# Optimization experiments

Hardware: AMD Instinct MI355X
Metric: run time of the kernel (lower is better)

The kernel has to match this reference:

```python
import jax, jax.numpy as jnp
import numpy as np

N_NODES = 10000
IN_SIZE, H_SIZE, OUT_SIZE = 512, 512, 64
N_EDGES = 163840


def gcn_conv(x, edge_index, W, b, n_nodes):
    """PyG-style GCNConv: add self-loops, sym-normalize, x @ W, scatter-add, + bias."""
    src, dst = edge_index[0], edge_index[1]
    loop = jnp.arange(n_nodes, dtype=src.dtype)
    src = jnp.concatenate([src, loop])
    dst = jnp.concatenate([dst, loop])
    # degree over destinations (self-loops included)
    deg = jax.ops.segment_sum(jnp.ones_like(dst, dtype=x.dtype), dst, num_segments=n_nodes)
    dinv = jnp.where(deg > 0, jax.lax.rsqrt(deg), 0.0)
    norm = dinv[src] * dinv[dst]                      # [E+N]
    h = x @ W                                          # [N, out]
    msg = h[src] * norm[:, None]                       # gather + scale
    out = jax.ops.segment_sum(msg, dst, num_segments=n_nodes)  # scatter-add
    return out + b


def setup_inputs() -> dict:
    key = jax.random.key(0)
    k = jax.random.split(key, 6)
    x = jax.random.normal(k[0], (N_NODES, IN_SIZE), dtype=jnp.float32)
    edge_index = jax.random.randint(k[1], (2, N_EDGES), 0, N_NODES, dtype=jnp.int64 if jax.config.read('jax_enable_x64') else jnp.int32)
    # Glorot-ish init for weights, zero bias (PyG default)
    W1 = jax.random.normal(k[2], (IN_SIZE, H_SIZE), dtype=jnp.float32) * (1.0 / np.sqrt(IN_SIZE))
    b1 = jnp.zeros((H_SIZE,), dtype=jnp.float32)
    W2 = jax.random.normal(k[3], (H_SIZE, OUT_SIZE), dtype=jnp.float32) * (1.0 / np.sqrt(H_SIZE))
    b2 = jnp.zeros((OUT_SIZE,), dtype=jnp.float32)
    return {"x": x, "edge_index": edge_index, "W1": W1, "b1": b1, "W2": W2, "b2": b2}


def reference(x, edge_index, W1, b1, W2, b2):
    n = x.shape[0]
    h = gcn_conv(x, edge_index, W1, b1, n)
    h = jax.nn.relu(h)
    h = gcn_conv(h, edge_index, W2, b2, n)
    return (h, jax.nn.log_softmax(h, axis=1))
```

## Files before the change

kernel.cpp:

```cpp
#include <hip/hip_runtime.h>
#include <math.h>

#define NN 10000
#define INF 512
#define HF  512
#define OF  64
#define NE  163840
#define MAXDEG 64

typedef __attribute__((ext_vector_type(8))) short bf16x8_t;
typedef __attribute__((ext_vector_type(4))) float f32x4_t;

__device__ inline ushort f2bf(float f) {
    unsigned u = __float_as_uint(f);
    u = (u + 0x7FFF + ((u >> 16) & 1)) >> 16;
    return (ushort)u;
}
__device__ inline float bf2f(ushort u) {
    return __uint_as_float(((unsigned)u) << 16);
}

#define CCB_X  2500
#define CCB_W1 2756
#define CCB_W2 2788
#define CCB_Z  2828
__global__ __launch_bounds__(256) void k_cvt(const float* __restrict__ X,
                                             ushort* __restrict__ Xb,
                                             const float* __restrict__ W1,
                                             ushort* __restrict__ W1T,
                                             const float* __restrict__ W2,
                                             ushort* __restrict__ W2T,
                                             int* __restrict__ gdeg) {
    __shared__ float tl[32][33];
    int b = blockIdx.x, t = threadIdx.x;
    if (b < CCB_X) {
        int i = (b * 256 + t) * 2;
        const float4* Xv = (const float4*)X;
        float4 v0 = Xv[i], v1 = Xv[i + 1];
        ushort4 o0, o1;
        o0.x = f2bf(v0.x); o0.y = f2bf(v0.y); o0.z = f2bf(v0.z); o0.w = f2bf(v0.w);
        o1.x = f2bf(v1.x); o1.y = f2bf(v1.y); o1.z = f2bf(v1.z); o1.w = f2bf(v1.w);
        ((ushort4*)Xb)[i] = o0;
        ((ushort4*)Xb)[i + 1] = o1;
    } else if (b < CCB_W2) {
        const float* W; ushort* WT; int N, tile;
        if (b < CCB_W1) { W = W1; WT = W1T; N = 512; tile = b - CCB_X; }
        else            { W = W2; WT = W2T; N = 64;  tile = b - CCB_W1; }
        int k0 = (tile & 15) * 32;
        int n0 = (tile >> 4) * 32;
        int tx = t & 31, ty = t >> 5;
#pragma unroll
        for (int i = 0; i < 4; i++)
            tl[ty + i * 8][tx] = W[(size_t)(k0 + ty + i * 8) * N + n0 + tx];
        __syncthreads();
#pragma unroll
        for (int i = 0; i < 4; i++)
            WT[(size_t)(n0 + ty + i * 8) * 512 + k0 + tx] = f2bf(tl[tx][ty + i * 8]);
    } else {
        int i = (b - CCB_W2) * 256 + t;
        if (i < NN) gdeg[i] = 0;
    }
}

#define LDA 72
#define GEMM_B 628
__global__ __launch_bounds__(256) void k_gemm_ell(const ushort* __restrict__ Xb,
                                                  const ushort* __restrict__ WT,
                                                  ushort* __restrict__ Y,
                                                  const int* __restrict__ src,
                                                  const int* __restrict__ dst,
                                                  int* __restrict__ gdeg,
                                                  int* __restrict__ ell, int E) {
    __shared__ ushort As[64 * LDA];
    __shared__ ushort Bs[128 * LDA];
    int b = blockIdx.x;
    int tid = threadIdx.x;
    if (b >= GEMM_B) {
        int e = (b - GEMM_B) * 256 + tid;
        if (e < E) {
            int s = src[e], d = dst[e];
            int r = atomicAdd(&gdeg[d], 1);
            if (r < MAXDEG) ell[d * MAXDEG + r] = s;
        }
        return;
    }
    int lane = tid & 63;
    int wave = tid >> 6;
    int m = lane & 15;
    int q = lane >> 4;
    int wr = wave >> 1;
    int wc = wave & 1;
    int row0 = (b % 157) * 64;
    int col0 = (b / 157) * 128;

    f32x4_t acc[2][4];
#pragma unroll
    for (int r = 0; r < 2; r++)
#pragma unroll
        for (int c = 0; c < 4; c++) acc[r][c] = (f32x4_t){0.f, 0.f, 0.f, 0.f};

    int srow = tid >> 3;
    int skk = (tid & 7) * 8;

    for (int kb = 0; kb < 512; kb += 64) {
#pragma unroll
        for (int c_ = 0; c_ < 2; c_++) {
            int row = srow + c_ * 32;
            int grow = row0 + row;
            bf16x8_t v = {0, 0, 0, 0, 0, 0, 0, 0};
            if (grow < NN)
                v = *(const bf16x8_t*)(Xb + (size_t)grow * 512 + kb + skk);
            *(bf16x8_t*)(As + row * LDA + skk) = v;
        }
#pragma unroll
        for (int c_ = 0; c_ < 4; c_++) {
            int n = srow + c_ * 32;
            bf16x8_t v = *(const bf16x8_t*)(WT + (size_t)(col0 + n) * 512 + kb + skk);
            *(bf16x8_t*)(Bs + n * LDA + skk) = v;
        }
        __syncthreads();
#pragma unroll
        for (int kc = 0; kc < 2; kc++) {
            bf16x8_t a[2], bb[4];
#pragma unroll
            for (int r = 0; r < 2; r++)
                a[r] = *(const bf16x8_t*)(As + (wr * 32 + r * 16 + m) * LDA + kc * 32 + q * 8);
#pragma unroll
            for (int c = 0; c < 4; c++)
                bb[c] = *(const bf16x8_t*)(Bs + (wc * 64 + c * 16 + m) * LDA + kc * 32 + q * 8);
#pragma unroll
            for (int r = 0; r < 2; r++)
#pragma unroll
                for (int c = 0; c < 4; c++)
                    acc[r][c] = __builtin_amdgcn_mfma_f32_16x16x32_bf16(a[r], bb[c], acc[r][c], 0, 0, 0);
        }
        __syncthreads();
    }
#pragma unroll
    for (int r = 0; r < 2; r++) {
#pragma unroll
        for (int c = 0; c < 4; c++) {
#pragma unroll
            for (int reg = 0; reg < 4; reg++) {
                int row = row0 + wr * 32 + r * 16 + q * 4 + reg;
                int col = col0 + wc * 64 + c * 16 + m;
                if (row < NN) Y[(size_t)row * 512 + col] = f2bf(acc[r][c][reg]);
            }
        }
    }
}

__global__ __launch_bounds__(256) void k_gemm64_mfma(const ushort* __restrict__ Ab,
                                                     const ushort* __restrict__ W2T,
                                                     ushort* __restrict__ Y) {
    __shared__ ushort As[64 * LDA];
    __shared__ ushort Bs[64 * LDA];
    int tid = threadIdx.x;
    int lane = tid & 63;
    int wave = tid >> 6;
    int m = lane & 15;
    int q = lane >> 4;
    int row0 = blockIdx.x * 64;

    f32x4_t acc[4];
#pragma unroll
    for (int c = 0; c < 4; c++) acc[c] = (f32x4_t){0.f, 0.f, 0.f, 0.f};

    int srow = tid >> 3;
    int skk = (tid & 7) * 8;

    for (int kb = 0; kb < 512; kb += 64) {
#pragma unroll
        for (int c_ = 0; c_ < 2; c_++) {
            int row = srow + c_ * 32;
            int grow = row0 + row;
            bf16x8_t v = {0, 0, 0, 0, 0, 0, 0, 0};
            if (grow < NN)
                v = *(const bf16x8_t*)(Ab + (size_t)grow * 512 + kb + skk);
            *(bf16x8_t*)(As + row * LDA + skk) = v;
            bf16x8_t wv = *(const bf16x8_t*)(W2T + (size_t)row * 512 + kb + skk);
            *(bf16x8_t*)(Bs + row * LDA + skk) = wv;
        }
        __syncthreads();
#pragma unroll
        for (int kc = 0; kc < 2; kc++) {
            bf16x8_t a = *(const bf16x8_t*)(As + (wave * 16 + m) * LDA + kc * 32 + q * 8);
#pragma unroll
            for (int c = 0; c < 4; c++) {
                bf16x8_t b = *(const bf16x8_t*)(Bs + (c * 16 + m) * LDA + kc * 32 + q * 8);
                acc[c] = __builtin_amdgcn_mfma_f32_16x16x32_bf16(a, b, acc[c], 0, 0, 0);
            }
        }
        __syncthreads();
    }
#pragma unroll
    for (int c = 0; c < 4; c++) {
#pragma unroll
        for (int reg = 0; reg < 4; reg++) {
            int row = row0 + wave * 16 + q * 4 + reg;
            int col = c * 16 + m;
            if (row < NN) Y[(size_t)row * 64 + col] = f2bf(acc[c][reg]);
        }
    }
}

__global__ __launch_bounds__(64) void k_agg1(const ushort* __restrict__ h1b,
                                             const int* __restrict__ gdeg,
                                             const int* __restrict__ ell,
                                             const float* __restrict__ b,
                                             ushort* __restrict__ a1b) {
    __shared__ int   sidx[64];
    __shared__ float swt[64];
    int bid = blockIdx.x;
    int slice = bid & 7;
    int v = bid >> 3;
    int t = threadIdx.x;
    int f = slice * 64 + t;
    int deg = gdeg[v]; if (deg > MAXDEG) deg = MAXDEG;
    float dv = rsqrtf((float)(deg + 1));
    int s = 0; float wt = 0.f;
    if (t < deg) {
        s = ell[v * MAXDEG + t];
        wt = rsqrtf((float)(gdeg[s] + 1)) * dv;
    }
    sidx[t] = s; swt[t] = wt;
    __syncthreads();

    float acc[8];
#pragma unroll
    for (int k = 0; k < 8; k++) acc[k] = 0.f;
    acc[0] = bf2f(h1b[(size_t)v * 512 + f]) * (dv * dv);

    int nr = (deg + 7) & ~7;
    for (int i = 0; i < nr; i += 8) {
        int   sK[8]; float wK[8];
#pragma unroll
        for (int k = 0; k < 8; k++) { sK[k] = sidx[i + k]; wK[k] = swt[i + k]; }
#pragma unroll
        for (int k = 0; k < 8; k++)
            acc[k] += bf2f(h1b[(size_t)sK[k] * 512 + f]) * wK[k];
    }
    float total = ((acc[0] + acc[1]) + (acc[2] + acc[3])) +
                  ((acc[4] + acc[5]) + (acc[6] + acc[7]));
    total += b[f];
    a1b[(size_t)v * 512 + f] = f2bf(total > 0.f ? total : 0.f);
}

__global__ __launch_bounds__(64) void k_agg2_lsm(const ushort* __restrict__ h2b,
                                                 const int* __restrict__ gdeg,
                                                 const int* __restrict__ ell,
                                                 const float* __restrict__ b,
                                                 float* __restrict__ out) {
    __shared__ int   sidx[64];
    __shared__ float swt[64];
    int v = blockIdx.x;
    int t = threadIdx.x;
    int deg = gdeg[v]; if (deg > MAXDEG) deg = MAXDEG;
    float dv = rsqrtf((float)(deg + 1));
    int s = 0; float wt = 0.f;
    if (t < deg) {
        s = ell[v * MAXDEG + t];
        wt = rsqrtf((float)(gdeg[s] + 1)) * dv;
    }
    sidx[t] = s; swt[t] = wt;
    __syncthreads();

    float acc[8];
#pragma unroll
    for (int k = 0; k < 8; k++) acc[k] = 0.f;
    acc[0] = bf2f(h2b[(size_t)v * 64 + t]) * (dv * dv);

    int nr = (deg + 7) & ~7;
    for (int i = 0; i < nr; i += 8) {
        int   sK[8]; float wK[8];
#pragma unroll
        for (int k = 0; k < 8; k++) { sK[k] = sidx[i + k]; wK[k] = swt[i + k]; }
#pragma unroll
        for (int k = 0; k < 8; k++)
            acc[k] += bf2f(h2b[(size_t)sK[k] * 64 + t]) * wK[k];
    }
    float h = ((acc[0] + acc[1]) + (acc[2] + acc[3])) +
              ((acc[4] + acc[5]) + (acc[6] + acc[7]));
    h += b[t];
    out[(size_t)v * 64 + t] = h;
    float m = h;
#pragma unroll
    for (int off = 32; off >= 1; off >>= 1) m = fmaxf(m, __shfl_xor(m, off, 64));
    float e = expf(h - m);
    float ssum = e;
#pragma unroll
    for (int off = 32; off >= 1; off >>= 1) ssum += __shfl_xor(ssum, off, 64);
    out[(size_t)NN * OF + (size_t)v * 64 + t] = h - m - logf(ssum);
}


extern "C" void kernel_launch(void* const* d_in, const int* in_sizes, int n_in,
                              void* d_out, int out_size, void* d_ws, size_t ws_size,
                              hipStream_t stream) {
    const float* x  = (const float*)d_in[0];
    const int*   ei = (const int*)d_in[1];
    const float* W1 = (const float*)d_in[2];
    const float* b1 = (const float*)d_in[3];
    const float* W2 = (const float*)d_in[4];
    const float* b2 = (const float*)d_in[5];
    float* out = (float*)d_out;

    int E = in_sizes[1] / 2;
    const int* src = ei;
    const int* dst = ei + E;

    char* w = (char*)d_ws;
    auto carve = [&](size_t bytes) {
        char* p = w;
        w += (bytes + 255) & ~size_t(255);
        return p;
    };
    ushort* Xb     = (ushort*)carve((size_t)NN * 512 * 2);
    ushort* h1b    = (ushort*)carve((size_t)NN * 512 * 2);
    ushort* a1b    = (ushort*)carve((size_t)NN * 512 * 2);
    ushort* h2b    = (ushort*)carve((size_t)NN * 64 * 2);
    ushort* W1Tb   = (ushort*)carve((size_t)512 * 512 * 2);
    ushort* W2Tb   = (ushort*)carve((size_t)64 * 512 * 2);
    int*   gdeg    = (int*)carve((size_t)NN * 4);
    int*   ell     = (int*)carve((size_t)NN * MAXDEG * 4);
    (void)ws_size;

    int fillB = (E + 255) / 256;
    k_cvt<<<CCB_Z, 256, 0, stream>>>(x, Xb, W1, W1Tb, W2, W2Tb, gdeg);
    k_gemm_ell<<<GEMM_B + fillB, 256, 0, stream>>>(Xb, W1Tb, h1b, src, dst,
                                                   gdeg, ell, E);
    k_agg1<<<NN * 8, 64, 0, stream>>>(h1b, gdeg, ell, b1, a1b);
    k_gemm64_mfma<<<(NN + 63) / 64, 256, 0, stream>>>(a1b, W2Tb, h2b);
    k_agg2_lsm<<<NN, 64, 0, stream>>>(h2b, gdeg, ell, b2, out);
}
```

Baseline: 145.7 us.

## Enlarge first GEMM tile to 128x128 and vectorize agg1 to two features per thread

The first-layer GEMM now uses 128x128 output tiles, with each wave computing a 64x64 sub-tile, which halves the number of GEMM blocks and raises the reuse of each loaded B tile. The layer-1 aggregation kernel now handles two adjacent bf16 features per thread with ushort2 loads and stores. That halves its block count and the per-block overhead of loading neighbour indices and computing degree weights. The larger GEMM tile raises accumulator register and LDS use, and its 316 blocks may underfill a 256-CU device compared with the previous 628.

```diff
diff --git a/kernel.cpp b/kernel.cpp
--- a/kernel.cpp
+++ b/kernel.cpp
@@ -63,7 +63,7 @@
 }
 
 #define LDA 72
-#define GEMM_B 628
+#define GEMM_B 316
 __global__ __launch_bounds__(256) void k_gemm_ell(const ushort* __restrict__ Xb,
                                                   const ushort* __restrict__ WT,
                                                   ushort* __restrict__ Y,
@@ -71,7 +71,7 @@
                                                   const int* __restrict__ dst,
                                                   int* __restrict__ gdeg,
                                                   int* __restrict__ ell, int E) {
-    __shared__ ushort As[64 * LDA];
+    __shared__ ushort As[128 * LDA];
     __shared__ ushort Bs[128 * LDA];
     int b = blockIdx.x;
     int tid = threadIdx.x;
@@ -90,12 +90,12 @@
     int q = lane >> 4;
     int wr = wave >> 1;
     int wc = wave & 1;
-    int row0 = (b % 157) * 64;
-    int col0 = (b / 157) * 128;
-
-    f32x4_t acc[2][4];
-#pragma unroll
-    for (int r = 0; r < 2; r++)
+    int row0 = (b % 79) * 128;
+    int col0 = (b / 79) * 128;
+
+    f32x4_t acc[4][4];
+#pragma unroll
+    for (int r = 0; r < 4; r++)
 #pragma unroll
         for (int c = 0; c < 4; c++) acc[r][c] = (f32x4_t){0.f, 0.f, 0.f, 0.f};
 
@@ -104,7 +104,7 @@
 
     for (int kb = 0; kb < 512; kb += 64) {
 #pragma unroll
-        for (int c_ = 0; c_ < 2; c_++) {
+        for (int c_ = 0; c_ < 4; c_++) {
             int row = srow + c_ * 32;
             int grow = row0 + row;
             bf16x8_t v = {0, 0, 0, 0, 0, 0, 0, 0};
@@ -121,15 +121,15 @@
         __syncthreads();
 #pragma unroll
         for (int kc = 0; kc < 2; kc++) {
-            bf16x8_t a[2], bb[4];
-#pragma unroll
-            for (int r = 0; r < 2; r++)
-                a[r] = *(const bf16x8_t*)(As + (wr * 32 + r * 16 + m) * LDA + kc * 32 + q * 8);
+            bf16x8_t a[4], bb[4];
+#pragma unroll
+            for (int r = 0; r < 4; r++)
+                a[r] = *(const bf16x8_t*)(As + (wr * 64 + r * 16 + m) * LDA + kc * 32 + q * 8);
 #pragma unroll
             for (int c = 0; c < 4; c++)
                 bb[c] = *(const bf16x8_t*)(Bs + (wc * 64 + c * 16 + m) * LDA + kc * 32 + q * 8);
 #pragma unroll
-            for (int r = 0; r < 2; r++)
+            for (int r = 0; r < 4; r++)
 #pragma unroll
                 for (int c = 0; c < 4; c++)
                     acc[r][c] = __builtin_amdgcn_mfma_f32_16x16x32_bf16(a[r], bb[c], acc[r][c], 0, 0, 0);
@@ -137,12 +137,12 @@
         __syncthreads();
     }
 #pragma unroll
-    for (int r = 0; r < 2; r++) {
+    for (int r = 0; r < 4; r++) {
 #pragma unroll
         for (int c = 0; c < 4; c++) {
 #pragma unroll
             for (int reg = 0; reg < 4; reg++) {
-                int row = row0 + wr * 32 + r * 16 + q * 4 + reg;
+                int row = row0 + wr * 64 + r * 16 + q * 4 + reg;
                 int col = col0 + wc * 64 + c * 16 + m;
                 if (row < NN) Y[(size_t)row * 512 + col] = f2bf(acc[r][c][reg]);
             }
@@ -212,10 +212,10 @@
     __shared__ int   sidx[64];
     __shared__ float swt[64];
     int bid = blockIdx.x;
-    int slice = bid & 7;
-    int v = bid >> 3;
+    int slice = bid & 3;
+    int v = bid >> 2;
     int t = threadIdx.x;
-    int f = slice * 64 + t;
+    int fb = slice * 128 + t * 2;
     int deg = gdeg[v]; if (deg > MAXDEG) deg = MAXDEG;
     float dv = rsqrtf((float)(deg + 1));
     int s = 0; float wt = 0.f;
@@ -226,24 +226,35 @@
     sidx[t] = s; swt[t] = wt;
     __syncthreads();
 
-    float acc[8];
-#pragma unroll
-    for (int k = 0; k < 8; k++) acc[k] = 0.f;
-    acc[0] = bf2f(h1b[(size_t)v * 512 + f]) * (dv * dv);
-
+    float ax[8], ay[8];
+#pragma unroll
+    for (int k = 0; k < 8; k++) { ax[k] = 0.f; ay[k] = 0.f; }
+    {
+        ushort2 u = *(const ushort2*)(h1b + (size_t)v * 512 + fb);
+        float dv2 = dv * dv;
+        ax[0] = bf2f(u.x) * dv2;
+        ay[0] = bf2f(u.y) * dv2;
+    }
     int nr = (deg + 7) & ~7;
     for (int i = 0; i < nr; i += 8) {
         int   sK[8]; float wK[8];
 #pragma unroll
         for (int k = 0; k < 8; k++) { sK[k] = sidx[i + k]; wK[k] = swt[i + k]; }
 #pragma unroll
-        for (int k = 0; k < 8; k++)
-            acc[k] += bf2f(h1b[(size_t)sK[k] * 512 + f]) * wK[k];
-    }
-    float total = ((acc[0] + acc[1]) + (acc[2] + acc[3])) +
-                  ((acc[4] + acc[5]) + (acc[6] + acc[7]));
-    total += b[f];
-    a1b[(size_t)v * 512 + f] = f2bf(total > 0.f ? total : 0.f);
+        for (int k = 0; k < 8; k++) {
+            ushort2 u = *(const ushort2*)(h1b + (size_t)sK[k] * 512 + fb);
+            ax[k] += bf2f(u.x) * wK[k];
+            ay[k] += bf2f(u.y) * wK[k];
+        }
+    }
+    float tx = ((ax[0] + ax[1]) + (ax[2] + ax[3])) + ((ax[4] + ax[5]) + (ax[6] + ax[7]));
+    float ty = ((ay[0] + ay[1]) + (ay[2] + ay[3])) + ((ay[4] + ay[5]) + (ay[6] + ay[7]));
+    tx += b[fb];
+    ty += b[fb + 1];
+    ushort2 o;
+    o.x = f2bf(tx > 0.f ? tx : 0.f);
+    o.y = f2bf(ty > 0.f ? ty : 0.f);
+    *(ushort2*)(a1b + (size_t)v * 512 + fb) = o;
 }
 
 __global__ __launch_bounds__(64) void k_agg2_lsm(const ushort* __restrict__ h2b,
@@ -329,7 +340,7 @@
     k_cvt<<<CCB_Z, 256, 0, stream>>>(x, Xb, W1, W1Tb, W2, W2Tb, gdeg);
     k_gemm_ell<<<GEMM_B + fillB, 256, 0, stream>>>(Xb, W1Tb, h1b, src, dst,
                                                    gdeg, ell, E);
-    k_agg1<<<NN * 8, 64, 0, stream>>>(h1b, gdeg, ell, b1, a1b);
+    k_agg1<<<NN * 4, 64, 0, stream>>>(h1b, gdeg, ell, b1, a1b);
     k_gemm64_mfma<<<(NN + 63) / 64, 256, 0, stream>>>(a1b, W2Tb, h2b);
     k_agg2_lsm<<<NN, 64, 0, stream>>>(h2b, gdeg, ell, b2, out);
 }
```

Result: faster. 141.2 us (-3.1%).
